# Kernel tuning notes

Hardware: AMD Instinct MI355X
Metric: run time of the kernel (lower is better)

## Reference

```python
import jax, jax.numpy as jnp
import numpy as np

NITERS = 5  # mean-field iterations (niters in __init__)


def setup_inputs() -> dict:
    key = jax.random.key(0)
    k1, k2 = jax.random.split(key)
    B, L, C, H, W = 2, 21, 3, 96, 96
    E0 = jax.random.normal(k1, (B, L, H, W), dtype=jnp.float32)
    Refs = jax.random.normal(k2, (B, C, H, W), dtype=jnp.float32)
    # potts_init: weight = ones(L,L) - eye(L)
    Mu_W = jnp.ones((L, L), dtype=jnp.float32) - jnp.eye(L, dtype=jnp.float32)
    return {"E0": E0, "Refs": Refs, "Mu_W": Mu_W}


def _affinity(Refs):
    # Reference-guided dense adjacency (BatchedAdjacency): row-normalized
    # Gaussian affinity on guide features, one N x N matrix per batch element.
    B, C, H, W = Refs.shape
    N = H * W
    f = Refs.reshape(B, C, N).transpose(0, 2, 1)  # [B, N, C]
    sq = jnp.sum(f * f, axis=-1)  # [B, N]
    D = sq[:, :, None] + sq[:, None, :] - 2.0 * jnp.einsum('bnc,bmc->bnm', f, f)
    A = jnp.exp(-0.5 * D)  # [B, N, N]
    return A / jnp.sum(A, axis=-1, keepdims=True)


def reference(E0, Refs, Mu_W):
    B, L, H, W = E0.shape
    N = H * W
    A = _affinity(Refs)  # computed once, reused every iteration
    E0f = E0.reshape(B, L, N)
    Qf = jax.nn.softmax(-E0f, axis=1)  # Q = softmax(-E0, dim=1)
    for _ in range(NITERS):
        # Potts compatibility transform (channel mixing): Mu(Q)
        M = jnp.einsum('kl,bln->bkn', Mu_W, Qf)
        # adjacency message passing: W(Mu(Q), Refs)
        msg = jnp.einsum('bnm,blm->bln', A, M)
        Qf = jax.nn.softmax(-(E0f + msg), axis=1)
    return Qf.reshape(B, L, H, W)
```

## Files before the change

### kernel.cpp

```cpp
#include <hip/hip_runtime.h>
#include <hip/hip_bf16.h>


#define BB 2
#define LL 21
#define LP (LL + 1)
#define NNPX 9216
#define NITERS 5
#define LOG2E 1.4426950408889634f

#define BARRIER() asm volatile("s_waitcnt lgkmcnt(0)\n\ts_barrier" ::: "memory")

typedef __attribute__((ext_vector_type(8))) short short8;
typedef __attribute__((ext_vector_type(4))) float f32x4;

static __device__ inline unsigned int pk_bf16(float a, float b) {
    __hip_bfloat162 h = __float22bfloat162_rn(make_float2(a, b));
    unsigned int u;
    __builtin_memcpy(&u, &h, 4);
    return u;
}

__global__ __launch_bounds__(256) void k_prep(
        const float* __restrict__ E0, const float* __restrict__ Refs,
        const float* __restrict__ Mu,
        float4* __restrict__ FN, float4* __restrict__ FS,
        __hip_bfloat16* __restrict__ MQ) {
    __shared__ float muS[LL * LL];
    for (int i = threadIdx.x; i < LL * LL; i += 256) muS[i] = Mu[i];
    __syncthreads();

    int idx = blockIdx.x * 256 + threadIdx.x;
    int b = idx / NNPX, n = idx % NNPX;

    const float* rb = Refs + (size_t)b * 3 * NNPX + n;
    float r0 = rb[0], r1 = rb[NNPX], r2 = rb[2 * NNPX];
    FN[idx] = make_float4(r0, r1, r2, 0.f);
    float g = -0.5f * (r0 * r0 + r1 * r1 + r2 * r2);
    FS[idx] = make_float4(g * LOG2E, r0 * LOG2E, r1 * LOG2E, r2 * LOG2E);

    const float* eb = E0 + (size_t)b * LL * NNPX + n;
    float x[LL];
    float mx = -1e30f;
    for (int l = 0; l < LL; ++l) { x[l] = -eb[(size_t)l * NNPX]; mx = fmaxf(mx, x[l]); }
    float s = 0.f;
    for (int l = 0; l < LL; ++l) { x[l] = __builtin_amdgcn_exp2f((x[l] - mx) * LOG2E); s += x[l]; }
    float rs = __builtin_amdgcn_rcpf(s);
    for (int l = 0; l < LL; ++l) x[l] *= rs;

    __hip_bfloat16* mq = MQ + (size_t)b * LL * NNPX + n;
    for (int k = 0; k < LL; ++k) {
        float a = 0.f;
        for (int l = 0; l < LL; ++l) a += muS[k * LL + l] * x[l];
        mq[(size_t)k * NNPX] = __float2bfloat16(a);
    }
}

__global__ __launch_bounds__(256, 4) void k_accum(
        const float4* __restrict__ FS, const float4* __restrict__ FN,
        const unsigned int* __restrict__ MQbf, float* __restrict__ Ppart, int S) {
    __shared__ __align__(16) unsigned short Wlds[64 * 72];
    __shared__ __align__(16) unsigned short Mlds[32 * 72];

    int t = threadIdx.x;
    int rb = blockIdx.x;
    int s  = blockIdx.y;
    int b  = rb / 144;
    int n0 = (rb % 144) * 64;
    int wv = t >> 6, lane = t & 63;
    int lr = lane & 15, g = lane >> 4;

    for (int i = t; i < 11 * 32; i += 256) {
        int r = 21 + (i >> 5), d = i & 31;
        ((unsigned int*)&Mlds[r * 72])[d] = (r == 21) ? 0x3F803F80u : 0u;
    }

    int mq = t & 15;
    int ng = t >> 4;
    float4 fnr[4];
    for (int i = 0; i < 4; ++i) fnr[i] = FN[b * NNPX + n0 + ng + 16 * i];

    const int T  = 144 / S;
    const int t0 = s * T;
    const float4* fsb = FS + (size_t)b * NNPX;
    const unsigned int* mqb = MQbf + (size_t)b * LL * (NNPX / 2);

    int sl0 = t >> 5, sm0 = t & 31;
    int sl1 = (t + 256) >> 5, sm1 = (t + 256) & 31;
    int sl2 = (t + 512) >> 5, sm2 = (t + 512) & 31;

    f32x4 acc0 = {0.f, 0.f, 0.f, 0.f};
    f32x4 acc1 = {0.f, 0.f, 0.f, 0.f};

    float4 fsA0, fsA1, fsA2, fsA3;
    unsigned int mrA0, mrA1, mrA2;

    int row = wv * 16 + lr;

    auto LOADA = [&](int tile) {
        int m0 = (t0 + tile) * 64;
        fsA0 = fsb[m0 + 4 * mq + 0]; fsA1 = fsb[m0 + 4 * mq + 1];
        fsA2 = fsb[m0 + 4 * mq + 2]; fsA3 = fsb[m0 + 4 * mq + 3];
        int mo0 = (t0 + tile) * 32;
        mrA0 = mqb[(size_t)sl0 * (NNPX / 2) + mo0 + sm0];
        mrA1 = mqb[(size_t)sl1 * (NNPX / 2) + mo0 + sm1];
        if (t < 160) mrA2 = mqb[(size_t)sl2 * (NNPX / 2) + mo0 + sm2];
    };
    auto STORE = [&]() {
        ((unsigned int*)&Mlds[sl0 * 72])[sm0] = mrA0;
        ((unsigned int*)&Mlds[sl1 * 72])[sm1] = mrA1;
        if (t < 160) ((unsigned int*)&Mlds[sl2 * 72])[sm2] = mrA2;
        #pragma unroll
        for (int i = 0; i < 4; ++i) {
            float4 f = fnr[i];
            float w0 = __builtin_amdgcn_exp2f(fsA0.x + f.x * fsA0.y + f.y * fsA0.z + f.z * fsA0.w);
            float w1 = __builtin_amdgcn_exp2f(fsA1.x + f.x * fsA1.y + f.y * fsA1.z + f.z * fsA1.w);
            float w2 = __builtin_amdgcn_exp2f(fsA2.x + f.x * fsA2.y + f.y * fsA2.z + f.z * fsA2.w);
            float w3 = __builtin_amdgcn_exp2f(fsA3.x + f.x * fsA3.y + f.y * fsA3.z + f.z * fsA3.w);
            uint2 pk;
            pk.x = pk_bf16(w0, w1);
            pk.y = pk_bf16(w2, w3);
            *(uint2*)&Wlds[(ng + 16 * i) * 72 + 4 * mq] = pk;
        }
    };
    auto MFMA = [&]() {
        short8 a0  = *(const short8*)&Wlds[row * 72 + g * 8];
        short8 a1  = *(const short8*)&Wlds[row * 72 + g * 8 + 32];
        short8 b00 = *(const short8*)&Mlds[lr * 72 + g * 8];
        short8 b01 = *(const short8*)&Mlds[lr * 72 + g * 8 + 32];
        short8 b10 = *(const short8*)&Mlds[(16 + lr) * 72 + g * 8];
        short8 b11 = *(const short8*)&Mlds[(16 + lr) * 72 + g * 8 + 32];
        acc0 = __builtin_amdgcn_mfma_f32_16x16x32_bf16(a0, b00, acc0, 0, 0, 0);
        acc0 = __builtin_amdgcn_mfma_f32_16x16x32_bf16(a1, b01, acc0, 0, 0, 0);
        acc1 = __builtin_amdgcn_mfma_f32_16x16x32_bf16(a0, b10, acc1, 0, 0, 0);
        acc1 = __builtin_amdgcn_mfma_f32_16x16x32_bf16(a1, b11, acc1, 0, 0, 0);
    };

    LOADA(0);

    for (int tt = 0; tt < T; ++tt) {
        BARRIER();
        STORE();
        if (tt + 1 < T) LOADA(tt + 1);
        BARRIER();
        MFMA();
    }

    int col = lane & 15, qr = lane >> 4;
    float* pp = Ppart + ((size_t)(s * BB + b) * LP) * NNPX;
    for (int r = 0; r < 4; ++r) {
        int n = n0 + wv * 16 + qr * 4 + r;
        pp[(size_t)col * NNPX + n] = acc0[r];
        if (col < LP - 16) pp[(size_t)(16 + col) * NNPX + n] = acc1[r];
    }
}

template <bool LAST>
__global__ __launch_bounds__(256) void k_softmax(
        const float* __restrict__ E0, const float* __restrict__ Ppart,
        const float* __restrict__ Mu,
        __hip_bfloat16* __restrict__ MQ, float* __restrict__ Out, int S) {
    __shared__ float muS[LL * LL];
    for (int i = threadIdx.x; i < LL * LL; i += 256) muS[i] = Mu[i];
    __syncthreads();

    int idx = blockIdx.x * 256 + threadIdx.x;
    int b = idx / NNPX, n = idx % NNPX;

    float P[LP];
    for (int l = 0; l < LP; ++l) P[l] = 0.f;
    for (int s = 0; s < S; ++s) {
        const float* pp = Ppart + ((size_t)(s * BB + b) * LP) * NNPX + n;
        for (int l = 0; l < LP; ++l) P[l] += pp[(size_t)l * NNPX];
    }
    float rinv = __builtin_amdgcn_rcpf(P[LL]);

    const float* eb = E0 + (size_t)b * LL * NNPX + n;
    float mx = -1e30f;
    for (int l = 0; l < LL; ++l) {
        P[l] = -(eb[(size_t)l * NNPX] + P[l] * rinv);
        mx = fmaxf(mx, P[l]);
    }
    float ssum = 0.f;
    for (int l = 0; l < LL; ++l) { P[l] = __builtin_amdgcn_exp2f((P[l] - mx) * LOG2E); ssum += P[l]; }
    float rs = __builtin_amdgcn_rcpf(ssum);
    for (int l = 0; l < LL; ++l) P[l] *= rs;

    if (LAST) {
        float* ob = Out + (size_t)b * LL * NNPX + n;
        for (int l = 0; l < LL; ++l) ob[(size_t)l * NNPX] = P[l];
    } else {
        __hip_bfloat16* mq = MQ + (size_t)b * LL * NNPX + n;
        for (int k = 0; k < LL; ++k) {
            float a = 0.f;
            for (int l = 0; l < LL; ++l) a += muS[k * LL + l] * P[l];
            mq[(size_t)k * NNPX] = __float2bfloat16(a);
        }
    }
}

extern "C" void kernel_launch(void* const* d_in, const int* in_sizes, int n_in,
                              void* d_out, int out_size, void* d_ws, size_t ws_size,
                              hipStream_t stream) {
    const float* E0   = (const float*)d_in[0];
    const float* Refs = (const float*)d_in[1];
    const float* Mu   = (const float*)d_in[2];
    float* out = (float*)d_out;

    char* w = (char*)d_ws;
    size_t off = 0;
    auto alloc = [&](size_t bytes) {
        void* p = w + off;
        off += (bytes + 255) & ~(size_t)255;
        return p;
    };
    float4* FN     = (float4*)alloc((size_t)BB * NNPX * sizeof(float4));
    float4* FS     = (float4*)alloc((size_t)BB * NNPX * sizeof(float4));
    __hip_bfloat16* MQbf = (__hip_bfloat16*)alloc((size_t)BB * LL * NNPX * sizeof(__hip_bfloat16));

    size_t per = (size_t)BB * LP * NNPX * sizeof(float);
    size_t avail = ws_size > off ? ws_size - off : 0;
    int Smax = (int)(avail / (per + 256));
    static const int divs[] = {8, 6, 4, 3, 2, 1};
    int S = 1;
    for (int i = 0; i < 6; ++i) if (divs[i] <= Smax) { S = divs[i]; break; }
    float* Ppart = (float*)alloc((size_t)S * per);

    k_prep<<<BB * NNPX / 256, 256, 0, stream>>>(E0, Refs, Mu, FN, FS, MQbf);
    for (int it = 0; it < NITERS; ++it) {
        k_accum<<<dim3(288, S), 256, 0, stream>>>(FS, FN, (const unsigned int*)MQbf, Ppart, S);
        if (it == NITERS - 1)
            k_softmax<true><<<BB * NNPX / 256, 256, 0, stream>>>(E0, Ppart, Mu, MQbf, out, S);
        else
            k_softmax<false><<<BB * NNPX / 256, 256, 0, stream>>>(E0, Ppart, Mu, MQbf, out, S);
    }
}
```

Before: 382.0 us.

## Load MQ operands directly into registers and XOR-swizzle the W tile in LDS

```diff
diff --git a/kernel.cpp b/kernel.cpp
--- a/kernel.cpp
+++ b/kernel.cpp
@@ -13,6 +13,7 @@
 
 typedef __attribute__((ext_vector_type(8))) short short8;
 typedef __attribute__((ext_vector_type(4))) float f32x4;
+typedef __attribute__((ext_vector_type(4))) unsigned int u32x4;
 
 static __device__ inline unsigned int pk_bf16(float a, float b) {
     __hip_bfloat162 h = __float22bfloat162_rn(make_float2(a, b));
@@ -58,9 +59,8 @@
 
 __global__ __launch_bounds__(256, 4) void k_accum(
         const float4* __restrict__ FS, const float4* __restrict__ FN,
-        const unsigned int* __restrict__ MQbf, float* __restrict__ Ppart, int S) {
-    __shared__ __align__(16) unsigned short Wlds[64 * 72];
-    __shared__ __align__(16) unsigned short Mlds[32 * 72];
+        const __hip_bfloat16* __restrict__ MQbf, float* __restrict__ Ppart, int S) {
+    __shared__ __align__(16) unsigned short Wlds[64 * 64];
 
     int t = threadIdx.x;
     int rb = blockIdx.x;
@@ -70,78 +70,84 @@
     int wv = t >> 6, lane = t & 63;
     int lr = lane & 15, g = lane >> 4;
 
-    for (int i = t; i < 11 * 32; i += 256) {
-        int r = 21 + (i >> 5), d = i & 31;
-        ((unsigned int*)&Mlds[r * 72])[d] = (r == 21) ? 0x3F803F80u : 0u;
-    }
-
     int mq = t & 15;
     int ng = t >> 4;
-    float4 fnr[4];
-    for (int i = 0; i < 4; ++i) fnr[i] = FN[b * NNPX + n0 + ng + 16 * i];
+    float fnx[4], fny[4], fnz[4];
+    #pragma unroll
+    for (int i = 0; i < 4; ++i) {
+        float4 v = FN[b * NNPX + n0 + ng + 16 * i];
+        fnx[i] = v.x; fny[i] = v.y; fnz[i] = v.z;
+    }
 
     const int T  = 144 / S;
     const int t0 = s * T;
     const float4* fsb = FS + (size_t)b * NNPX;
-    const unsigned int* mqb = MQbf + (size_t)b * LL * (NNPX / 2);
-
-    int sl0 = t >> 5, sm0 = t & 31;
-    int sl1 = (t + 256) >> 5, sm1 = (t + 256) & 31;
-    int sl2 = (t + 512) >> 5, sm2 = (t + 512) & 31;
+    const __hip_bfloat16* mqb = MQbf + (size_t)b * LL * NNPX;
 
     f32x4 acc0 = {0.f, 0.f, 0.f, 0.f};
     f32x4 acc1 = {0.f, 0.f, 0.f, 0.f};
 
+    short8 ones8;
+    {
+        u32x4 o = {0x3F803F80u, 0x3F803F80u, 0x3F803F80u, 0x3F803F80u};
+        ones8 = __builtin_bit_cast(short8, o);
+    }
+
+    int r1 = 16 + lr; if (r1 > 20) r1 = 20;
+
+    int row = wv * 16 + lr;
+    int ia0 = row * 64 + ((g ^ (lr & 7)) << 3);
+    int ia1 = row * 64 + (((g + 4) ^ (lr & 7)) << 3);
+    int wq = ng & 7;
+    int wcol = (((mq >> 1) ^ wq) << 3) + ((mq & 1) << 2);
+
     float4 fsA0, fsA1, fsA2, fsA3;
-    unsigned int mrA0, mrA1, mrA2;
-
-    int row = wv * 16 + lr;
-
-    auto LOADA = [&](int tile) {
+    short8 b00, b01, b10, b11;
+
+    auto LOADFS = [&](int tile) {
         int m0 = (t0 + tile) * 64;
         fsA0 = fsb[m0 + 4 * mq + 0]; fsA1 = fsb[m0 + 4 * mq + 1];
         fsA2 = fsb[m0 + 4 * mq + 2]; fsA3 = fsb[m0 + 4 * mq + 3];
-        int mo0 = (t0 + tile) * 32;
-        mrA0 = mqb[(size_t)sl0 * (NNPX / 2) + mo0 + sm0];
-        mrA1 = mqb[(size_t)sl1 * (NNPX / 2) + mo0 + sm1];
-        if (t < 160) mrA2 = mqb[(size_t)sl2 * (NNPX / 2) + mo0 + sm2];
+    };
+    auto LOADB = [&](int tile) {
+        const __hip_bfloat16* p0 = mqb + (size_t)lr * NNPX + (t0 + tile) * 64 + g * 8;
+        b00 = *(const short8*)p0;
+        b01 = *(const short8*)(p0 + 32);
+        const __hip_bfloat16* p1 = mqb + (size_t)r1 * NNPX + (t0 + tile) * 64 + g * 8;
+        b10 = *(const short8*)p1;
+        b11 = *(const short8*)(p1 + 32);
     };
     auto STORE = [&]() {
-        ((unsigned int*)&Mlds[sl0 * 72])[sm0] = mrA0;
-        ((unsigned int*)&Mlds[sl1 * 72])[sm1] = mrA1;
-        if (t < 160) ((unsigned int*)&Mlds[sl2 * 72])[sm2] = mrA2;
         #pragma unroll
         for (int i = 0; i < 4; ++i) {
-            float4 f = fnr[i];
-            float w0 = __builtin_amdgcn_exp2f(fsA0.x + f.x * fsA0.y + f.y * fsA0.z + f.z * fsA0.w);
-            float w1 = __builtin_amdgcn_exp2f(fsA1.x + f.x * fsA1.y + f.y * fsA1.z + f.z * fsA1.w);
-            float w2 = __builtin_amdgcn_exp2f(fsA2.x + f.x * fsA2.y + f.y * fsA2.z + f.z * fsA2.w);
-            float w3 = __builtin_amdgcn_exp2f(fsA3.x + f.x * fsA3.y + f.y * fsA3.z + f.z * fsA3.w);
+            float w0 = __builtin_amdgcn_exp2f(fsA0.x + fnx[i] * fsA0.y + fny[i] * fsA0.z + fnz[i] * fsA0.w);
+            float w1 = __builtin_amdgcn_exp2f(fsA1.x + fnx[i] * fsA1.y + fny[i] * fsA1.z + fnz[i] * fsA1.w);
+            float w2 = __builtin_amdgcn_exp2f(fsA2.x + fnx[i] * fsA2.y + fny[i] * fsA2.z + fnz[i] * fsA2.w);
+            float w3 = __builtin_amdgcn_exp2f(fsA3.x + fnx[i] * fsA3.y + fny[i] * fsA3.z + fnz[i] * fsA3.w);
             uint2 pk;
             pk.x = pk_bf16(w0, w1);
             pk.y = pk_bf16(w2, w3);
-            *(uint2*)&Wlds[(ng + 16 * i) * 72 + 4 * mq] = pk;
+            *(uint2*)&Wlds[(ng + 16 * i) * 64 + wcol] = pk;
         }
     };
     auto MFMA = [&]() {
-        short8 a0  = *(const short8*)&Wlds[row * 72 + g * 8];
-        short8 a1  = *(const short8*)&Wlds[row * 72 + g * 8 + 32];
-        short8 b00 = *(const short8*)&Mlds[lr * 72 + g * 8];
-        short8 b01 = *(const short8*)&Mlds[lr * 72 + g * 8 + 32];
-        short8 b10 = *(const short8*)&Mlds[(16 + lr) * 72 + g * 8];
-        short8 b11 = *(const short8*)&Mlds[(16 + lr) * 72 + g * 8 + 32];
+        short8 a0 = *(const short8*)&Wlds[ia0];
+        short8 a1 = *(const short8*)&Wlds[ia1];
+        short8 v10 = b10, v11 = b11;
+        if (lr == 5) { v10 = ones8; v11 = ones8; }
         acc0 = __builtin_amdgcn_mfma_f32_16x16x32_bf16(a0, b00, acc0, 0, 0, 0);
         acc0 = __builtin_amdgcn_mfma_f32_16x16x32_bf16(a1, b01, acc0, 0, 0, 0);
-        acc1 = __builtin_amdgcn_mfma_f32_16x16x32_bf16(a0, b10, acc1, 0, 0, 0);
-        acc1 = __builtin_amdgcn_mfma_f32_16x16x32_bf16(a1, b11, acc1, 0, 0, 0);
-    };
-
-    LOADA(0);
+        acc1 = __builtin_amdgcn_mfma_f32_16x16x32_bf16(a0, v10, acc1, 0, 0, 0);
+        acc1 = __builtin_amdgcn_mfma_f32_16x16x32_bf16(a1, v11, acc1, 0, 0, 0);
+    };
+
+    LOADFS(0);
 
     for (int tt = 0; tt < T; ++tt) {
         BARRIER();
+        LOADB(tt);
         STORE();
-        if (tt + 1 < T) LOADA(tt + 1);
+        if (tt + 1 < T) LOADFS(tt + 1);
         BARRIER();
         MFMA();
     }
@@ -228,7 +234,7 @@
 
     k_prep<<<BB * NNPX / 256, 256, 0, stream>>>(E0, Refs, Mu, FN, FS, MQbf);
     for (int it = 0; it < NITERS; ++it) {
-        k_accum<<<dim3(288, S), 256, 0, stream>>>(FS, FN, (const unsigned int*)MQbf, Ppart, S);
+        k_accum<<<dim3(288, S), 256, 0, stream>>>(FS, FN, MQbf, Ppart, S);
         if (it == NITERS - 1)
             k_softmax<true><<<BB * NNPX / 256, 256, 0, stream>>>(E0, Ppart, Mu, MQbf, out, S);
         else
```

Result: slower. 592.1 us (+55.0%).

## Double k_accum row tile to 128 and XOR-swizzle the W LDS tile

Applied to the files above, without the earlier changes.

```diff
diff --git a/kernel.cpp b/kernel.cpp
--- a/kernel.cpp
+++ b/kernel.cpp
@@ -59,14 +59,14 @@
 __global__ __launch_bounds__(256, 4) void k_accum(
         const float4* __restrict__ FS, const float4* __restrict__ FN,
         const unsigned int* __restrict__ MQbf, float* __restrict__ Ppart, int S) {
-    __shared__ __align__(16) unsigned short Wlds[64 * 72];
+    __shared__ __align__(16) unsigned short Wlds[2][64 * 64];
     __shared__ __align__(16) unsigned short Mlds[32 * 72];
 
     int t = threadIdx.x;
     int rb = blockIdx.x;
     int s  = blockIdx.y;
-    int b  = rb / 144;
-    int n0 = (rb % 144) * 64;
+    int b  = rb / 72;
+    int n0 = (rb % 72) * 128;
     int wv = t >> 6, lane = t & 63;
     int lr = lane & 15, g = lane >> 4;
 
@@ -77,8 +77,12 @@
 
     int mq = t & 15;
     int ng = t >> 4;
-    float4 fnr[4];
-    for (int i = 0; i < 4; ++i) fnr[i] = FN[b * NNPX + n0 + ng + 16 * i];
+    float fnx[8], fny[8], fnz[8];
+    #pragma unroll
+    for (int i = 0; i < 8; ++i) {
+        float4 v = FN[b * NNPX + n0 + ng + 16 * i];
+        fnx[i] = v.x; fny[i] = v.y; fnz[i] = v.z;
+    }
 
     const int T  = 144 / S;
     const int t0 = s * T;
@@ -89,15 +93,24 @@
     int sl1 = (t + 256) >> 5, sm1 = (t + 256) & 31;
     int sl2 = (t + 512) >> 5, sm2 = (t + 512) & 31;
 
-    f32x4 acc0 = {0.f, 0.f, 0.f, 0.f};
-    f32x4 acc1 = {0.f, 0.f, 0.f, 0.f};
+    f32x4 acc0  = {0.f, 0.f, 0.f, 0.f};
+    f32x4 acc1  = {0.f, 0.f, 0.f, 0.f};
+    f32x4 acc0b = {0.f, 0.f, 0.f, 0.f};
+    f32x4 acc1b = {0.f, 0.f, 0.f, 0.f};
+
+    int wcol = ((((mq >> 1) ^ (ng & 7)) << 3) + ((mq & 1) << 2));
+
+    int half  = wv >> 1;
+    int rloc  = (wv & 1) * 32 + lr;
+    int ia0 = rloc * 64 + ((g ^ (lr & 7)) << 3);
+    int ia1 = rloc * 64 + (((g + 4) ^ (lr & 7)) << 3);
+    int ib0 = (rloc + 16) * 64 + ((g ^ (lr & 7)) << 3);
+    int ib1 = (rloc + 16) * 64 + (((g + 4) ^ (lr & 7)) << 3);
 
     float4 fsA0, fsA1, fsA2, fsA3;
     unsigned int mrA0, mrA1, mrA2;
 
-    int row = wv * 16 + lr;
-
-    auto LOADA = [&](int tile) {
+    auto LOAD = [&](int tile) {
         int m0 = (t0 + tile) * 64;
         fsA0 = fsb[m0 + 4 * mq + 0]; fsA1 = fsb[m0 + 4 * mq + 1];
         fsA2 = fsb[m0 + 4 * mq + 2]; fsA3 = fsb[m0 + 4 * mq + 3];
@@ -111,37 +124,43 @@
         ((unsigned int*)&Mlds[sl1 * 72])[sm1] = mrA1;
         if (t < 160) ((unsigned int*)&Mlds[sl2 * 72])[sm2] = mrA2;
         #pragma unroll
-        for (int i = 0; i < 4; ++i) {
-            float4 f = fnr[i];
-            float w0 = __builtin_amdgcn_exp2f(fsA0.x + f.x * fsA0.y + f.y * fsA0.z + f.z * fsA0.w);
-            float w1 = __builtin_amdgcn_exp2f(fsA1.x + f.x * fsA1.y + f.y * fsA1.z + f.z * fsA1.w);
-            float w2 = __builtin_amdgcn_exp2f(fsA2.x + f.x * fsA2.y + f.y * fsA2.z + f.z * fsA2.w);
-            float w3 = __builtin_amdgcn_exp2f(fsA3.x + f.x * fsA3.y + f.y * fsA3.z + f.z * fsA3.w);
+        for (int i = 0; i < 8; ++i) {
+            float w0 = __builtin_amdgcn_exp2f(fsA0.x + fnx[i] * fsA0.y + fny[i] * fsA0.z + fnz[i] * fsA0.w);
+            float w1 = __builtin_amdgcn_exp2f(fsA1.x + fnx[i] * fsA1.y + fny[i] * fsA1.z + fnz[i] * fsA1.w);
+            float w2 = __builtin_amdgcn_exp2f(fsA2.x + fnx[i] * fsA2.y + fny[i] * fsA2.z + fnz[i] * fsA2.w);
+            float w3 = __builtin_amdgcn_exp2f(fsA3.x + fnx[i] * fsA3.y + fny[i] * fsA3.z + fnz[i] * fsA3.w);
             uint2 pk;
             pk.x = pk_bf16(w0, w1);
             pk.y = pk_bf16(w2, w3);
-            *(uint2*)&Wlds[(ng + 16 * i) * 72 + 4 * mq] = pk;
+            int r = ng + 16 * i;
+            *(uint2*)&Wlds[i >> 2][(r & 63) * 64 + wcol] = pk;
         }
     };
     auto MFMA = [&]() {
-        short8 a0  = *(const short8*)&Wlds[row * 72 + g * 8];
-        short8 a1  = *(const short8*)&Wlds[row * 72 + g * 8 + 32];
         short8 b00 = *(const short8*)&Mlds[lr * 72 + g * 8];
         short8 b01 = *(const short8*)&Mlds[lr * 72 + g * 8 + 32];
         short8 b10 = *(const short8*)&Mlds[(16 + lr) * 72 + g * 8];
         short8 b11 = *(const short8*)&Mlds[(16 + lr) * 72 + g * 8 + 32];
-        acc0 = __builtin_amdgcn_mfma_f32_16x16x32_bf16(a0, b00, acc0, 0, 0, 0);
-        acc0 = __builtin_amdgcn_mfma_f32_16x16x32_bf16(a1, b01, acc0, 0, 0, 0);
-        acc1 = __builtin_amdgcn_mfma_f32_16x16x32_bf16(a0, b10, acc1, 0, 0, 0);
-        acc1 = __builtin_amdgcn_mfma_f32_16x16x32_bf16(a1, b11, acc1, 0, 0, 0);
-    };
-
-    LOADA(0);
+        short8 a0 = *(const short8*)&Wlds[half][ia0];
+        short8 a1 = *(const short8*)&Wlds[half][ia1];
+        short8 c0 = *(const short8*)&Wlds[half][ib0];
+        short8 c1 = *(const short8*)&Wlds[half][ib1];
+        acc0  = __builtin_amdgcn_mfma_f32_16x16x32_bf16(a0, b00, acc0,  0, 0, 0);
+        acc0  = __builtin_amdgcn_mfma_f32_16x16x32_bf16(a1, b01, acc0,  0, 0, 0);
+        acc1  = __builtin_amdgcn_mfma_f32_16x16x32_bf16(a0, b10, acc1,  0, 0, 0);
+        acc1  = __builtin_amdgcn_mfma_f32_16x16x32_bf16(a1, b11, acc1,  0, 0, 0);
+        acc0b = __builtin_amdgcn_mfma_f32_16x16x32_bf16(c0, b00, acc0b, 0, 0, 0);
+        acc0b = __builtin_amdgcn_mfma_f32_16x16x32_bf16(c1, b01, acc0b, 0, 0, 0);
+        acc1b = __builtin_amdgcn_mfma_f32_16x16x32_bf16(c0, b10, acc1b, 0, 0, 0);
+        acc1b = __builtin_amdgcn_mfma_f32_16x16x32_bf16(c1, b11, acc1b, 0, 0, 0);
+    };
+
+    LOAD(0);
 
     for (int tt = 0; tt < T; ++tt) {
         BARRIER();
         STORE();
-        if (tt + 1 < T) LOADA(tt + 1);
+        if (tt + 1 < T) LOAD(tt + 1);
         BARRIER();
         MFMA();
     }
@@ -149,9 +168,13 @@
     int col = lane & 15, qr = lane >> 4;
     float* pp = Ppart + ((size_t)(s * BB + b) * LP) * NNPX;
     for (int r = 0; r < 4; ++r) {
-        int n = n0 + wv * 16 + qr * 4 + r;
+        int n = n0 + wv * 32 + qr * 4 + r;
         pp[(size_t)col * NNPX + n] = acc0[r];
-        if (col < LP - 16) pp[(size_t)(16 + col) * NNPX + n] = acc1[r];
+        pp[(size_t)col * NNPX + n + 16] = acc0b[r];
+        if (col < LP - 16) {
+            pp[(size_t)(16 + col) * NNPX + n] = acc1[r];
+            pp[(size_t)(16 + col) * NNPX + n + 16] = acc1b[r];
+        }
     }
 }
 
@@ -228,7 +251,7 @@
 
     k_prep<<<BB * NNPX / 256, 256, 0, stream>>>(E0, Refs, Mu, FN, FS, MQbf);
     for (int it = 0; it < NITERS; ++it) {
-        k_accum<<<dim3(288, S), 256, 0, stream>>>(FS, FN, (const unsigned int*)MQbf, Ppart, S);
+        k_accum<<<dim3(144, S), 256, 0, stream>>>(FS, FN, (const unsigned int*)MQbf, Ppart, S);
         if (it == NITERS - 1)
             k_softmax<true><<<BB * NNPX / 256, 256, 0, stream>>>(E0, Ppart, Mu, MQbf, out, S);
         else
```

Result: slower. 404.0 us (+5.8%).

## Use atomic accumulation for split-K partials and swizzle W tile in LDS

Applied to the files above, without the earlier changes.

```diff
diff --git a/kernel.cpp b/kernel.cpp
--- a/kernel.cpp
+++ b/kernel.cpp
@@ -7,6 +7,7 @@
 #define LP (LL + 1)
 #define NNPX 9216
 #define NITERS 5
+#define MSPLIT 8
 #define LOG2E 1.4426950408889634f
 
 #define BARRIER() asm volatile("s_waitcnt lgkmcnt(0)\n\ts_barrier" ::: "memory")
@@ -58,8 +59,8 @@
 
 __global__ __launch_bounds__(256, 4) void k_accum(
         const float4* __restrict__ FS, const float4* __restrict__ FN,
-        const unsigned int* __restrict__ MQbf, float* __restrict__ Ppart, int S) {
-    __shared__ __align__(16) unsigned short Wlds[64 * 72];
+        const unsigned int* __restrict__ MQbf, float* __restrict__ Ppart) {
+    __shared__ __align__(16) unsigned short Wlds[64 * 64];
     __shared__ __align__(16) unsigned short Mlds[32 * 72];
 
     int t = threadIdx.x;
@@ -77,10 +78,14 @@
 
     int mq = t & 15;
     int ng = t >> 4;
-    float4 fnr[4];
-    for (int i = 0; i < 4; ++i) fnr[i] = FN[b * NNPX + n0 + ng + 16 * i];
-
-    const int T  = 144 / S;
+    float fnx[4], fny[4], fnz[4];
+    #pragma unroll
+    for (int i = 0; i < 4; ++i) {
+        float4 v = FN[b * NNPX + n0 + ng + 16 * i];
+        fnx[i] = v.x; fny[i] = v.y; fnz[i] = v.z;
+    }
+
+    const int T  = 144 / MSPLIT;
     const int t0 = s * T;
     const float4* fsb = FS + (size_t)b * NNPX;
     const unsigned int* mqb = MQbf + (size_t)b * LL * (NNPX / 2);
@@ -92,12 +97,16 @@
     f32x4 acc0 = {0.f, 0.f, 0.f, 0.f};
     f32x4 acc1 = {0.f, 0.f, 0.f, 0.f};
 
+    int wcol = (((mq >> 1) ^ (ng & 7)) << 3) + ((mq & 1) << 2);
+
+    int row = wv * 16 + lr;
+    int ia0 = row * 64 + ((g ^ (lr & 7)) << 3);
+    int ia1 = row * 64 + (((g + 4) ^ (lr & 7)) << 3);
+
     float4 fsA0, fsA1, fsA2, fsA3;
     unsigned int mrA0, mrA1, mrA2;
 
-    int row = wv * 16 + lr;
-
-    auto LOADA = [&](int tile) {
+    auto LOAD = [&](int tile) {
         int m0 = (t0 + tile) * 64;
         fsA0 = fsb[m0 + 4 * mq + 0]; fsA1 = fsb[m0 + 4 * mq + 1];
         fsA2 = fsb[m0 + 4 * mq + 2]; fsA3 = fsb[m0 + 4 * mq + 3];
@@ -112,20 +121,19 @@
         if (t < 160) ((unsigned int*)&Mlds[sl2 * 72])[sm2] = mrA2;
         #pragma unroll
         for (int i = 0; i < 4; ++i) {
-            float4 f = fnr[i];
-            float w0 = __builtin_amdgcn_exp2f(fsA0.x + f.x * fsA0.y + f.y * fsA0.z + f.z * fsA0.w);
-            float w1 = __builtin_amdgcn_exp2f(fsA1.x + f.x * fsA1.y + f.y * fsA1.z + f.z * fsA1.w);
-            float w2 = __builtin_amdgcn_exp2f(fsA2.x + f.x * fsA2.y + f.y * fsA2.z + f.z * fsA2.w);
-            float w3 = __builtin_amdgcn_exp2f(fsA3.x + f.x * fsA3.y + f.y * fsA3.z + f.z * fsA3.w);
+            float w0 = __builtin_amdgcn_exp2f(fsA0.x + fnx[i] * fsA0.y + fny[i] * fsA0.z + fnz[i] * fsA0.w);
+            float w1 = __builtin_amdgcn_exp2f(fsA1.x + fnx[i] * fsA1.y + fny[i] * fsA1.z + fnz[i] * fsA1.w);
+            float w2 = __builtin_amdgcn_exp2f(fsA2.x + fnx[i] * fsA2.y + fny[i] * fsA2.z + fnz[i] * fsA2.w);
+            float w3 = __builtin_amdgcn_exp2f(fsA3.x + fnx[i] * fsA3.y + fny[i] * fsA3.z + fnz[i] * fsA3.w);
             uint2 pk;
             pk.x = pk_bf16(w0, w1);
             pk.y = pk_bf16(w2, w3);
-            *(uint2*)&Wlds[(ng + 16 * i) * 72 + 4 * mq] = pk;
+            *(uint2*)&Wlds[(ng + 16 * i) * 64 + wcol] = pk;
         }
     };
     auto MFMA = [&]() {
-        short8 a0  = *(const short8*)&Wlds[row * 72 + g * 8];
-        short8 a1  = *(const short8*)&Wlds[row * 72 + g * 8 + 32];
+        short8 a0  = *(const short8*)&Wlds[ia0];
+        short8 a1  = *(const short8*)&Wlds[ia1];
         short8 b00 = *(const short8*)&Mlds[lr * 72 + g * 8];
         short8 b01 = *(const short8*)&Mlds[lr * 72 + g * 8 + 32];
         short8 b10 = *(const short8*)&Mlds[(16 + lr) * 72 + g * 8];
@@ -136,22 +144,22 @@
         acc1 = __builtin_amdgcn_mfma_f32_16x16x32_bf16(a1, b11, acc1, 0, 0, 0);
     };
 
-    LOADA(0);
+    LOAD(0);
 
     for (int tt = 0; tt < T; ++tt) {
         BARRIER();
         STORE();
-        if (tt + 1 < T) LOADA(tt + 1);
+        if (tt + 1 < T) LOAD(tt + 1);
         BARRIER();
         MFMA();
     }
 
     int col = lane & 15, qr = lane >> 4;
-    float* pp = Ppart + ((size_t)(s * BB + b) * LP) * NNPX;
+    float* pp = Ppart + (size_t)b * LP * NNPX;
     for (int r = 0; r < 4; ++r) {
         int n = n0 + wv * 16 + qr * 4 + r;
-        pp[(size_t)col * NNPX + n] = acc0[r];
-        if (col < LP - 16) pp[(size_t)(16 + col) * NNPX + n] = acc1[r];
+        atomicAdd(&pp[(size_t)col * NNPX + n], acc0[r]);
+        if (col < LP - 16) atomicAdd(&pp[(size_t)(16 + col) * NNPX + n], acc1[r]);
     }
 }
 
@@ -159,7 +167,7 @@
 __global__ __launch_bounds__(256) void k_softmax(
         const float* __restrict__ E0, const float* __restrict__ Ppart,
         const float* __restrict__ Mu,
-        __hip_bfloat16* __restrict__ MQ, float* __restrict__ Out, int S) {
+        __hip_bfloat16* __restrict__ MQ, float* __restrict__ Out) {
     __shared__ float muS[LL * LL];
     for (int i = threadIdx.x; i < LL * LL; i += 256) muS[i] = Mu[i];
     __syncthreads();
@@ -167,18 +175,14 @@
     int idx = blockIdx.x * 256 + threadIdx.x;
     int b = idx / NNPX, n = idx % NNPX;
 
-    float P[LP];
-    for (int l = 0; l < LP; ++l) P[l] = 0.f;
-    for (int s = 0; s < S; ++s) {
-        const float* pp = Ppart + ((size_t)(s * BB + b) * LP) * NNPX + n;
-        for (int l = 0; l < LP; ++l) P[l] += pp[(size_t)l * NNPX];
-    }
-    float rinv = __builtin_amdgcn_rcpf(P[LL]);
+    const float* pp = Ppart + (size_t)b * LP * NNPX + n;
+    float rinv = __builtin_amdgcn_rcpf(pp[(size_t)LL * NNPX]);
 
     const float* eb = E0 + (size_t)b * LL * NNPX + n;
+    float P[LL];
     float mx = -1e30f;
     for (int l = 0; l < LL; ++l) {
-        P[l] = -(eb[(size_t)l * NNPX] + P[l] * rinv);
+        P[l] = -(eb[(size_t)l * NNPX] + pp[(size_t)l * NNPX] * rinv);
         mx = fmaxf(mx, P[l]);
     }
     float ssum = 0.f;
@@ -217,21 +221,16 @@
     float4* FN     = (float4*)alloc((size_t)BB * NNPX * sizeof(float4));
     float4* FS     = (float4*)alloc((size_t)BB * NNPX * sizeof(float4));
     __hip_bfloat16* MQbf = (__hip_bfloat16*)alloc((size_t)BB * LL * NNPX * sizeof(__hip_bfloat16));
-
-    size_t per = (size_t)BB * LP * NNPX * sizeof(float);
-    size_t avail = ws_size > off ? ws_size - off : 0;
-    int Smax = (int)(avail / (per + 256));
-    static const int divs[] = {8, 6, 4, 3, 2, 1};
-    int S = 1;
-    for (int i = 0; i < 6; ++i) if (divs[i] <= Smax) { S = divs[i]; break; }
-    float* Ppart = (float*)alloc((size_t)S * per);
+    size_t psz = (size_t)BB * LP * NNPX * sizeof(float);
+    float* Ppart = (float*)alloc(psz);
 
     k_prep<<<BB * NNPX / 256, 256, 0, stream>>>(E0, Refs, Mu, FN, FS, MQbf);
     for (int it = 0; it < NITERS; ++it) {
-        k_accum<<<dim3(288, S), 256, 0, stream>>>(FS, FN, (const unsigned int*)MQbf, Ppart, S);
+        hipMemsetAsync(Ppart, 0, psz, stream);
+        k_accum<<<dim3(288, MSPLIT), 256, 0, stream>>>(FS, FN, (const unsigned int*)MQbf, Ppart);
         if (it == NITERS - 1)
-            k_softmax<true><<<BB * NNPX / 256, 256, 0, stream>>>(E0, Ppart, Mu, MQbf, out, S);
+            k_softmax<true><<<BB * NNPX / 256, 256, 0, stream>>>(E0, Ppart, Mu, MQbf, out);
         else
-            k_softmax<false><<<BB * NNPX / 256, 256, 0, stream>>>(E0, Ppart, Mu, MQbf, out, S);
-    }
-}
+            k_softmax<false><<<BB * NNPX / 256, 256, 0, stream>>>(E0, Ppart, Mu, MQbf, out);
+    }
+}
```

New measurement: 423.8 us. 1.11x slower.
